# Performance work log

Hardware: AMD Instinct MI355X
Metric: run time of the kernel (lower is better)

The kernel has to match this reference:

```python
import jax, jax.numpy as jnp
import numpy as np

B, N, D, E = 64, 512, 256, 524288
VOCAB, NTYPES = 50000, 8
NUM_NODES = B * N


def setup_inputs() -> dict:
    key = jax.random.key(0)
    ks = jax.random.split(key, 20)
    p = lambda k, shape: jax.random.normal(k, shape, jnp.float32) * 0.05
    return {
        'x_tokens': jax.random.randint(ks[0], (NUM_NODES,), 0, VOCAB),
        'word_type': jax.random.randint(ks[1], (NUM_NODES,), 0, NTYPES),
        'edge_index': jax.random.randint(ks[2], (2, E), 0, NUM_NODES),
        'edge_attr': jax.random.uniform(ks[3], (E,), jnp.float32),
        'mask_pad': jnp.ones((B, N, 1), jnp.float32),
        'mask_score': jnp.zeros((B, N), jnp.float32),
        'emb_table': p(ks[4], (VOCAB, D)),
        'wt_table': p(ks[5], (NTYPES, D)),
        'W_w': p(ks[6], (D, D)), 'b_w': jnp.zeros((D,), jnp.float32),
        'W_g1': p(ks[7], (D, D)), 'b_g1': jnp.zeros((D,), jnp.float32),
        'W_g2': p(ks[8], (D, D)), 'b_g2': jnp.zeros((D,), jnp.float32),
        'W_p1': p(ks[9], (D, D)), 'b_p1': jnp.zeros((D,), jnp.float32),
        'W_p2': p(ks[10], (D, 1)),
        'Wih_x': p(ks[11], (4 * D, D)), 'Whh_x': p(ks[12], (4 * D, D)),
        'bih_x': jnp.zeros((4 * D,), jnp.float32), 'bhh_x': jnp.zeros((4 * D,), jnp.float32),
        'Wih_g': p(ks[13], (4 * D, D)), 'Whh_g': p(ks[14], (4 * D, D)),
        'bih_g': jnp.zeros((4 * D,), jnp.float32), 'bhh_g': jnp.zeros((4 * D,), jnp.float32),
    }


def _lstm_cell(x, h, c, Wih, Whh, bih, bhh):
    g = x @ Wih.T + h @ Whh.T + (bih + bhh)
    i, f, gg, o = jnp.split(g, 4, axis=-1)  # torch gate order: i, f, g, o
    c = jax.nn.sigmoid(f) * c + jax.nn.sigmoid(i) * jnp.tanh(gg)
    h = jax.nn.sigmoid(o) * jnp.tanh(c)
    return h, c


def _lstm_last(x0, x1, Wih, Whh, bih, bhh):
    # batch_first LSTM over seq-len-2 input; return last hidden output
    z = jnp.zeros_like(x0)
    h, c = _lstm_cell(x0, z, z, Wih, Whh, bih, bhh)
    h, _ = _lstm_cell(x1, h, c, Wih, Whh, bih, bhh)
    return h


def _gcn(x, src, dst, ew, W, b):
    # PyG GCNConv with edge_weight: add self-loops (w=1), symmetric norm
    deg = jax.ops.segment_sum(ew, dst, NUM_NODES) + 1.0
    dinv = jax.lax.rsqrt(deg)
    norm = dinv[src] * ew * dinv[dst]  # [E]
    xw = x @ W                         # [NUM_NODES, D]
    out = jax.ops.segment_sum(norm[:, None] * xw[src], dst, NUM_NODES)
    out = out + (dinv * dinv)[:, None] * xw  # self-loop contribution
    return out + b


def _pool(x2d, W_p1, b_p1, W_p2, mask_score):
    x3 = x2d.reshape(B, N, D)
    h = jnp.tanh(x3 @ W_p1 + b_p1)
    score = (h @ W_p2)[..., 0] + mask_score  # [B, N]
    alpha = jax.nn.softmax(score, axis=-1)
    return jnp.sum(alpha[..., None] * x3, axis=1)  # [B, D]


def reference(x_tokens, word_type, edge_index, edge_attr, mask_pad, mask_score,
              emb_table, wt_table, W_w, b_w, W_g1, b_g1, W_g2, b_g2,
              W_p1, b_p1, W_p2, Wih_x, Whh_x, bih_x, bhh_x,
              Wih_g, Whh_g, bih_g, bhh_g):
    src, dst = edge_index[0], edge_index[1]
    x = emb_table[x_tokens] + wt_table[word_type]  # use_wordtype == True
    x = x @ W_w + b_w
    x1_mid = _gcn(x, src, dst, edge_attr, W_g1, b_g1)
    x1 = _lstm_last(x, x1_mid, Wih_x, Whh_x, bih_x, bhh_x)
    g1 = _pool(x1, W_p1, b_p1, W_p2, mask_score)
    x2_mid = _gcn(x1, src, dst, edge_attr, W_g2, b_g2)
    x2 = _lstm_last(x1, x2_mid, Wih_x, Whh_x, bih_x, bhh_x)
    g2 = _pool(x2, W_p1, b_p1, W_p2, mask_score)
    graph_out = _lstm_last(g1, g2, Wih_g, Whh_g, bih_g, bhh_g)  # [B, D]
    x_out = jnp.tanh(x2).reshape(B, N, D) * mask_pad
    return x_out, graph_out
```

## Files before the change

### kernel.cpp

```cpp
#include <hip/hip_runtime.h>
#include <hip/hip_bf16.h>
#include <math.h>

#define NODES 32768
#define DD 256
#define NE 524288
#define BATCH 64
#define SEQ 512

typedef __attribute__((ext_vector_type(8))) short short8v;
typedef __attribute__((ext_vector_type(4))) float f32x4;
typedef unsigned short u16;

__device__ __forceinline__ float sigf(float x) { return 1.0f / (1.0f + expf(-x)); }
__device__ __forceinline__ float bfu(u16 u) {
    unsigned int x = ((unsigned int)u) << 16;
    float f;
    __builtin_memcpy(&f, &x, 4);
    return f;
}
__device__ __forceinline__ u16 f2b(float f) {
    __hip_bfloat16 h = __float2bfloat16(f);
    u16 u;
    __builtin_memcpy(&u, &h, 2);
    return u;
}
__device__ __forceinline__ void split_store(float v, u16* __restrict__ hi, u16* __restrict__ lo, int idx) {
    u16 h = f2b(v);
    hi[idx] = h;
    lo[idx] = f2b(v - bfu(h));
}

__global__ __launch_bounds__(256) void wsplitT(const float* __restrict__ W,
                                               u16* __restrict__ h, u16* __restrict__ l) {
    int n = blockIdx.x, k = threadIdx.x;
    split_store(W[k * 256 + n], h, l, n * 256 + k);
}
__global__ __launch_bounds__(256) void wsplit(const float* __restrict__ W,
                                              u16* __restrict__ h, u16* __restrict__ l) {
    int i = blockIdx.x * 256 + threadIdx.x;
    split_store(W[i], h, l, i);
}

__global__ __launch_bounds__(256) void embed_split(const int* __restrict__ tok,
                                                   const int* __restrict__ wty,
                                                   const float* __restrict__ emb,
                                                   const float* __restrict__ wt,
                                                   u16* __restrict__ xh, u16* __restrict__ xl) {
    int i = blockIdx.x, d = threadIdx.x;
    float v = emb[tok[i] * DD + d] + wt[wty[i] * DD + d];
    split_store(v, xh, xl, i * DD + d);
}

template <bool TANH>
__global__ __launch_bounds__(256) void mfma_gemm(const u16* __restrict__ Ah, const u16* __restrict__ Al,
                                                 const u16* __restrict__ Bh, const u16* __restrict__ Bl,
                                                 const float* __restrict__ bias,
                                                 u16* __restrict__ Chi, u16* __restrict__ Clo) {
    const int l = threadIdx.x & 63, w = threadIdx.x >> 6;
    const int m0 = blockIdx.x * 64, n0 = w * 64;
    const int lr = l & 15, lk = (l >> 4) * 8;
    f32x4 acc[4][4];
#pragma unroll
    for (int mi = 0; mi < 4; ++mi)
#pragma unroll
        for (int ni = 0; ni < 4; ++ni) acc[mi][ni] = (f32x4){0.f, 0.f, 0.f, 0.f};

    const u16* APtr[3] = {Ah, Ah, Al};
    const u16* BPtr[3] = {Bh, Bl, Bh};
    for (int term = 0; term < 3; ++term) {
        const u16* A = APtr[term];
        const u16* B = BPtr[term];
#pragma unroll
        for (int kb = 0; kb < 8; ++kb) {
            int ka = kb * 32 + lk;
            short8v a[4], b[4];
#pragma unroll
            for (int mi = 0; mi < 4; ++mi)
                a[mi] = *(const short8v*)&A[(m0 + mi * 16 + lr) * 256 + ka];
#pragma unroll
            for (int ni = 0; ni < 4; ++ni)
                b[ni] = *(const short8v*)&B[(n0 + ni * 16 + lr) * 256 + ka];
#pragma unroll
            for (int mi = 0; mi < 4; ++mi)
#pragma unroll
                for (int ni = 0; ni < 4; ++ni)
                    acc[mi][ni] = __builtin_amdgcn_mfma_f32_16x16x32_bf16(a[mi], b[ni], acc[mi][ni], 0, 0, 0);
        }
    }
#pragma unroll
    for (int mi = 0; mi < 4; ++mi)
#pragma unroll
        for (int ni = 0; ni < 4; ++ni) {
            int col = n0 + ni * 16 + lr;
            float bs = bias[col];
#pragma unroll
            for (int r = 0; r < 4; ++r) {
                int row = m0 + mi * 16 + (l >> 4) * 4 + r;
                float v = acc[mi][ni][r] + bs;
                if (TANH) v = tanhf(v);
                split_store(v, Chi, Clo, row * 256 + col);
            }
        }
}

template <bool FIRST>
__global__ __launch_bounds__(256) void mfma_lstm(const u16* __restrict__ Xh, const u16* __restrict__ Xl,
                                                 const u16* __restrict__ Hh, const u16* __restrict__ Hl,
                                                 const u16* __restrict__ Wih_h, const u16* __restrict__ Wih_l,
                                                 const u16* __restrict__ Whh_h, const u16* __restrict__ Whh_l,
                                                 const float* __restrict__ bih, const float* __restrict__ bhh,
                                                 const float* __restrict__ c_in, float* __restrict__ c_out,
                                                 u16* __restrict__ Ohi, u16* __restrict__ Olo) {
    __shared__ float lds[4][64][65];
    const int l = threadIdx.x & 63, g = threadIdx.x >> 6;
    const int m0 = blockIdx.x * 64, d0 = blockIdx.y * 64;
    const int lr = l & 15, lk = (l >> 4) * 8;
    f32x4 acc[4][4];
#pragma unroll
    for (int mi = 0; mi < 4; ++mi)
#pragma unroll
        for (int ni = 0; ni < 4; ++ni) acc[mi][ni] = (f32x4){0.f, 0.f, 0.f, 0.f};

    const int npass = FIRST ? 1 : 2;
    for (int pass = 0; pass < npass; ++pass) {
        const u16* Ih = pass ? Hh : Xh;
        const u16* Il = pass ? Hl : Xl;
        const u16* Wh = pass ? Whh_h : Wih_h;
        const u16* Wl = pass ? Whh_l : Wih_l;
        const u16* APtr[3] = {Ih, Ih, Il};
        const u16* BPtr[3] = {Wh, Wl, Wh};
        for (int term = 0; term < 3; ++term) {
            const u16* A = APtr[term];
            const u16* B = BPtr[term];
#pragma unroll
            for (int kb = 0; kb < 8; ++kb) {
                int ka = kb * 32 + lk;
                short8v a[4], b[4];
#pragma unroll
                for (int mi = 0; mi < 4; ++mi)
                    a[mi] = *(const short8v*)&A[(m0 + mi * 16 + lr) * 256 + ka];
#pragma unroll
                for (int ni = 0; ni < 4; ++ni)
                    b[ni] = *(const short8v*)&B[(g * 256 + d0 + ni * 16 + lr) * 256 + ka];
#pragma unroll
                for (int mi = 0; mi < 4; ++mi)
#pragma unroll
                    for (int ni = 0; ni < 4; ++ni)
                        acc[mi][ni] = __builtin_amdgcn_mfma_f32_16x16x32_bf16(a[mi], b[ni], acc[mi][ni], 0, 0, 0);
            }
        }
    }
#pragma unroll
    for (int mi = 0; mi < 4; ++mi)
#pragma unroll
        for (int ni = 0; ni < 4; ++ni)
#pragma unroll
            for (int r = 0; r < 4; ++r)
                lds[g][mi * 16 + (l >> 4) * 4 + r][ni * 16 + lr] = acc[mi][ni][r];
    __syncthreads();
#pragma unroll 4
    for (int rep = 0; rep < 16; ++rep) {
        int idx = rep * 256 + threadIdx.x;
        int ml = idx >> 6, dl = idx & 63;
        int row = m0 + ml, d = d0 + dl;
        float gi = lds[0][ml][dl] + bih[d] + bhh[d];
        float gf = lds[1][ml][dl] + bih[256 + d] + bhh[256 + d];
        float gg = lds[2][ml][dl] + bih[512 + d] + bhh[512 + d];
        float go = lds[3][ml][dl] + bih[768 + d] + bhh[768 + d];
        float cprev = FIRST ? 0.0f : c_in[row * 256 + d];
        float cv = sigf(gf) * cprev + sigf(gi) * tanhf(gg);
        float hv = sigf(go) * tanhf(cv);
        c_out[row * 256 + d] = cv;
        split_store(hv, Ohi, Olo, row * 256 + d);
    }
}

template <bool FIRST>
__global__ __launch_bounds__(256) void lstm_gemm(const float* __restrict__ X,
                                                 const float* __restrict__ H,
                                                 const float* __restrict__ Wih,
                                                 const float* __restrict__ Whh,
                                                 const float* __restrict__ bih,
                                                 const float* __restrict__ bhh,
                                                 const float* __restrict__ c_in,
                                                 float* __restrict__ c_out,
                                                 float* __restrict__ h_out, int M) {
    __shared__ float As[16][68];
    __shared__ float Bs[4][16][68];
    const int m0 = blockIdx.x * 64;
    const int n0 = blockIdx.y * 64;
    const int t = threadIdx.x;
    const int ty = t >> 4, tx = t & 15;
    const int lm = t >> 2;
    const int lk4 = (t & 3) * 4;
    float acc[4][4][4] = {};
    const int npass = FIRST ? 1 : 2;
    for (int pass = 0; pass < npass; ++pass) {
        const float* Ain = pass ? H : X;
        const float* W = pass ? Whh : Wih;
        for (int k0 = 0; k0 < 256; k0 += 16) {
            float4 av = *(const float4*)&Ain[(m0 + lm) * 256 + k0 + lk4];
            float4 w0 = *(const float4*)&W[(0 * 256 + n0 + lm) * 256 + k0 + lk4];
            float4 w1 = *(const float4*)&W[(1 * 256 + n0 + lm) * 256 + k0 + lk4];
            float4 w2 = *(const float4*)&W[(2 * 256 + n0 + lm) * 256 + k0 + lk4];
            float4 w3 = *(const float4*)&W[(3 * 256 + n0 + lm) * 256 + k0 + lk4];
            __syncthreads();
            As[lk4 + 0][lm] = av.x; As[lk4 + 1][lm] = av.y;
            As[lk4 + 2][lm] = av.z; As[lk4 + 3][lm] = av.w;
            Bs[0][lk4 + 0][lm] = w0.x; Bs[0][lk4 + 1][lm] = w0.y;
            Bs[0][lk4 + 2][lm] = w0.z; Bs[0][lk4 + 3][lm] = w0.w;
            Bs[1][lk4 + 0][lm] = w1.x; Bs[1][lk4 + 1][lm] = w1.y;
            Bs[1][lk4 + 2][lm] = w1.z; Bs[1][lk4 + 3][lm] = w1.w;
            Bs[2][lk4 + 0][lm] = w2.x; Bs[2][lk4 + 1][lm] = w2.y;
            Bs[2][lk4 + 2][lm] = w2.z; Bs[2][lk4 + 3][lm] = w2.w;
            Bs[3][lk4 + 0][lm] = w3.x; Bs[3][lk4 + 1][lm] = w3.y;
            Bs[3][lk4 + 2][lm] = w3.z; Bs[3][lk4 + 3][lm] = w3.w;
            __syncthreads();
#pragma unroll
            for (int kk = 0; kk < 16; ++kk) {
                float4 a = *(const float4*)&As[kk][ty * 4];
                float av4[4] = {a.x, a.y, a.z, a.w};
#pragma unroll
                for (int gg = 0; gg < 4; ++gg) {
                    float4 b = *(const float4*)&Bs[gg][kk][tx * 4];
                    float bv4[4] = {b.x, b.y, b.z, b.w};
#pragma unroll
                    for (int i = 0; i < 4; ++i)
#pragma unroll
                        for (int j = 0; j < 4; ++j)
                            acc[gg][i][j] = fmaf(av4[i], bv4[j], acc[gg][i][j]);
                }
            }
        }
    }
#pragma unroll
    for (int i = 0; i < 4; ++i) {
        int r = m0 + ty * 4 + i;
#pragma unroll
        for (int j = 0; j < 4; ++j) {
            int dcol = n0 + tx * 4 + j;
            float gi = acc[0][i][j] + bih[dcol] + bhh[dcol];
            float gf = acc[1][i][j] + bih[256 + dcol] + bhh[256 + dcol];
            float gg = acc[2][i][j] + bih[512 + dcol] + bhh[512 + dcol];
            float go = acc[3][i][j] + bih[768 + dcol] + bhh[768 + dcol];
            float cprev = FIRST ? 0.0f : c_in[r * 256 + dcol];
            float cv = sigf(gf) * cprev + sigf(gi) * tanhf(gg);
            float hv = sigf(go) * tanhf(cv);
            c_out[r * 256 + dcol] = cv;
            h_out[r * 256 + dcol] = hv;
        }
    }
}

__global__ __launch_bounds__(256) void csr_init(int* __restrict__ counts, float* __restrict__ deg) {
    int i = blockIdx.x * 256 + threadIdx.x;
    counts[i] = 0;
    deg[i] = 1.0f;
}
__global__ __launch_bounds__(256) void csr_hist(const int* __restrict__ dst,
                                                const float* __restrict__ ew,
                                                int* __restrict__ counts,
                                                float* __restrict__ deg) {
    int e = blockIdx.x * 256 + threadIdx.x;
    int d = dst[e];
    atomicAdd(&counts[d], 1);
    atomicAdd(&deg[d], ew[e]);
}
__global__ __launch_bounds__(256) void csr_dinv(float* __restrict__ deg) {
    int i = blockIdx.x * 256 + threadIdx.x;
    deg[i] = 1.0f / sqrtf(deg[i]);
}
__global__ __launch_bounds__(256) void csr_scan(const int* __restrict__ counts,
                                                int* __restrict__ offs,
                                                int* __restrict__ cursor) {
    __shared__ int part[256];
    int t = threadIdx.x;
    int base = t * 128;
    int s = 0;
    for (int k = 0; k < 128; ++k) s += counts[base + k];
    part[t] = s;
    __syncthreads();
    for (int off = 1; off < 256; off <<= 1) {
        int v = part[t];
        int add = (t >= off) ? part[t - off] : 0;
        __syncthreads();
        part[t] = v + add;
        __syncthreads();
    }
    int run = part[t] - s;
    for (int k = 0; k < 128; ++k) {
        int c = counts[base + k];
        offs[base + k] = run;
        cursor[base + k] = run;
        run += c;
    }
    if (t == 255) offs[NODES] = run;
}
__global__ __launch_bounds__(256) void csr_fill(const int* __restrict__ src,
                                                const int* __restrict__ dst,
                                                const float* __restrict__ ew,
                                                const float* __restrict__ dinv,
                                                int* __restrict__ cursor,
                                                int* __restrict__ es,
                                                float* __restrict__ en) {
    int e = blockIdx.x * 256 + threadIdx.x;
    int s = src[e], d = dst[e];
    int pos = atomicAdd(&cursor[d], 1);
    es[pos] = s;
    en[pos] = dinv[s] * ew[e] * dinv[d];
}

__global__ __launch_bounds__(256) void gcn_gather(const u16* __restrict__ xh, const u16* __restrict__ xl,
                                                  const int* __restrict__ offs,
                                                  const int* __restrict__ es,
                                                  const float* __restrict__ en,
                                                  const float* __restrict__ dinv,
                                                  u16* __restrict__ oh, u16* __restrict__ ol) {
    int i = blockIdx.x, d = threadIdx.x;
    float di = dinv[i];
    float acc = di * di * (bfu(xh[i * DD + d]) + bfu(xl[i * DD + d]));
    int a = offs[i], b = offs[i + 1];
    for (int j = a; j < b; ++j) {
        int s = es[j];
        float w = en[j];
        acc += w * (bfu(xh[s * DD + d]) + bfu(xl[s * DD + d]));
    }
    split_store(acc, oh, ol, i * DD + d);
}

__global__ __launch_bounds__(256) void score_kernel(const u16* __restrict__ hh, const u16* __restrict__ hl,
                                                    const float* __restrict__ Wp2,
                                                    const float* __restrict__ mask_score,
                                                    float* __restrict__ score) {
    int m = blockIdx.x * 4 + (threadIdx.x >> 6);
    int l = threadIdx.x & 63;
    ushort4 a = *(const ushort4*)&hh[m * DD + l * 4];
    ushort4 b = *(const ushort4*)&hl[m * DD + l * 4];
    float4 w = *(const float4*)&Wp2[l * 4];
    float d = (bfu(a.x) + bfu(b.x)) * w.x + (bfu(a.y) + bfu(b.y)) * w.y +
              (bfu(a.z) + bfu(b.z)) * w.z + (bfu(a.w) + bfu(b.w)) * w.w;
#pragma unroll
    for (int off = 32; off; off >>= 1) d += __shfl_down(d, off);
    if (l == 0) score[m] = d + mask_score[m];
}

__global__ __launch_bounds__(256) void pool_kernel(const u16* __restrict__ xh, const u16* __restrict__ xl,
                                                   const float* __restrict__ score,
                                                   float* __restrict__ gout) {
    int b = blockIdx.x;
    int t = threadIdx.x;
    __shared__ float sal[512];
    __shared__ float wred[4];
    __shared__ float sbc[2];
    int lane = t & 63, wv = t >> 6;
    float s0 = score[b * SEQ + t];
    float s1 = score[b * SEQ + 256 + t];
    float m = fmaxf(s0, s1);
#pragma unroll
    for (int off = 32; off; off >>= 1) m = fmaxf(m, __shfl_down(m, off));
    if (lane == 0) wred[wv] = m;
    __syncthreads();
    if (t == 0) sbc[0] = fmaxf(fmaxf(wred[0], wred[1]), fmaxf(wred[2], wred[3]));
    __syncthreads();
    float mx = sbc[0];
    float e0 = expf(s0 - mx), e1 = expf(s1 - mx);
    sal[t] = e0;
    sal[t + 256] = e1;
    float sm = e0 + e1;
#pragma unroll
    for (int off = 32; off; off >>= 1) sm += __shfl_down(sm, off);
    __syncthreads();
    if (lane == 0) wred[wv] = sm;
    __syncthreads();
    if (t == 0) sbc[1] = wred[0] + wred[1] + wred[2] + wred[3];
    __syncthreads();
    float inv = 1.0f / sbc[1];
    float accv = 0.0f;
    size_t base = (size_t)b * SEQ * DD + t;
    for (int n = 0; n < SEQ; ++n)
        accv += sal[n] * (bfu(xh[base + (size_t)n * DD]) + bfu(xl[base + (size_t)n * DD]));
    gout[b * DD + t] = accv * inv;
}

__global__ __launch_bounds__(256) void final_kernel(const u16* __restrict__ xh, const u16* __restrict__ xl,
                                                    const float* __restrict__ mask_pad,
                                                    float* __restrict__ out) {
    int i = blockIdx.x, d = threadIdx.x;
    float v = bfu(xh[i * DD + d]) + bfu(xl[i * DD + d]);
    out[i * DD + d] = tanhf(v) * mask_pad[i];
}

extern "C" void kernel_launch(void* const* d_in, const int* in_sizes, int n_in,
                              void* d_out, int out_size, void* d_ws, size_t ws_size,
                              hipStream_t stream) {
    const int* x_tokens = (const int*)d_in[0];
    const int* word_type = (const int*)d_in[1];
    const int* edge_src = (const int*)d_in[2];
    const int* edge_dst = edge_src + NE;
    const float* edge_attr = (const float*)d_in[3];
    const float* mask_pad = (const float*)d_in[4];
    const float* mask_score = (const float*)d_in[5];
    const float* emb = (const float*)d_in[6];
    const float* wt = (const float*)d_in[7];
    const float* W_w = (const float*)d_in[8];
    const float* b_w = (const float*)d_in[9];
    const float* W_g1 = (const float*)d_in[10];
    const float* b_g1 = (const float*)d_in[11];
    const float* W_g2 = (const float*)d_in[12];
    const float* b_g2 = (const float*)d_in[13];
    const float* W_p1 = (const float*)d_in[14];
    const float* b_p1 = (const float*)d_in[15];
    const float* W_p2 = (const float*)d_in[16];
    const float* Wih_x = (const float*)d_in[17];
    const float* Whh_x = (const float*)d_in[18];
    const float* bih_x = (const float*)d_in[19];
    const float* bhh_x = (const float*)d_in[20];
    const float* Wih_g = (const float*)d_in[21];
    const float* Whh_g = (const float*)d_in[22];
    const float* bih_g = (const float*)d_in[23];
    const float* bhh_g = (const float*)d_in[24];

    float* out = (float*)d_out;
    char* ws = (char*)d_ws;

    int* counts = (int*)ws;
    int* cursor = counts + NODES;
    int* offs = cursor + NODES;
    float* dinv = (float*)(offs + NODES + 64);
    float* score = dinv + NODES;
    float* g1 = score + NODES;
    float* g2 = g1 + BATCH * DD;
    float* hg = g2 + BATCH * DD;
    float* cg = hg + BATCH * DD;
    int* es = (int*)(cg + BATCH * DD);
    float* en = (float*)(es + NE);
    u16* wsm = (u16*)(en + NE);
    u16* wwTh = wsm;               u16* wwTl = wwTh + 65536;
    u16* wg1h = wwTl + 65536;      u16* wg1l = wg1h + 65536;
    u16* wg2h = wg1l + 65536;      u16* wg2l = wg2h + 65536;
    u16* wp1h = wg2l + 65536;      u16* wp1l = wp1h + 65536;
    u16* wihh = wp1l + 65536;      u16* wihl = wihh + 262144;
    u16* whhh = wihl + 262144;     u16* whhl = whhh + 262144;

    const size_t NDf = (size_t)NODES * DD;
    u16* base = (u16*)(ws + (8u << 20));
    u16* S1h = base;               u16* S1l = S1h + NDf;
    u16* S2h = S1l + NDf;          u16* S2l = S2h + NDf;
    u16* S3h = S2l + NDf;          u16* S3l = S3h + NDf;
    float* OUTB = out;

    dim3 blk(256);
    dim3 gemmGrid(NODES / 64);
    dim3 lstmGrid(NODES / 64, 4);

    csr_init<<<NODES / 256, blk, 0, stream>>>(counts, dinv);
    csr_hist<<<NE / 256, blk, 0, stream>>>(edge_dst, edge_attr, counts, dinv);
    csr_dinv<<<NODES / 256, blk, 0, stream>>>(dinv);
    csr_scan<<<1, blk, 0, stream>>>(counts, offs, cursor);
    csr_fill<<<NE / 256, blk, 0, stream>>>(edge_src, edge_dst, edge_attr, dinv, cursor, es, en);

    wsplitT<<<256, blk, 0, stream>>>(W_w, wwTh, wwTl);
    wsplitT<<<256, blk, 0, stream>>>(W_g1, wg1h, wg1l);
    wsplitT<<<256, blk, 0, stream>>>(W_g2, wg2h, wg2l);
    wsplitT<<<256, blk, 0, stream>>>(W_p1, wp1h, wp1l);
    wsplit<<<1024, blk, 0, stream>>>(Wih_x, wihh, wihl);
    wsplit<<<1024, blk, 0, stream>>>(Whh_x, whhh, whhl);

    embed_split<<<NODES, blk, 0, stream>>>(x_tokens, word_type, emb, wt, S1h, S1l);
    mfma_gemm<false><<<gemmGrid, blk, 0, stream>>>(S1h, S1l, wwTh, wwTl, b_w, S2h, S2l);
    gcn_gather<<<NODES, blk, 0, stream>>>(S2h, S2l, offs, es, en, dinv, S1h, S1l);
    mfma_gemm<false><<<gemmGrid, blk, 0, stream>>>(S1h, S1l, wg1h, wg1l, b_g1, S3h, S3l);
    mfma_lstm<true><<<lstmGrid, blk, 0, stream>>>(S2h, S2l, nullptr, nullptr, wihh, wihl, whhh, whhl,
                                                  bih_x, bhh_x, nullptr, OUTB, S1h, S1l);
    mfma_lstm<false><<<lstmGrid, blk, 0, stream>>>(S3h, S3l, S1h, S1l, wihh, wihl, whhh, whhl,
                                                   bih_x, bhh_x, OUTB, OUTB, S2h, S2l);
    mfma_gemm<true><<<gemmGrid, blk, 0, stream>>>(S2h, S2l, wp1h, wp1l, b_p1, S3h, S3l);
    score_kernel<<<NODES / 4, blk, 0, stream>>>(S3h, S3l, W_p2, mask_score, score);
    pool_kernel<<<BATCH, blk, 0, stream>>>(S2h, S2l, score, g1);
    gcn_gather<<<NODES, blk, 0, stream>>>(S2h, S2l, offs, es, en, dinv, S1h, S1l);
    mfma_gemm<false><<<gemmGrid, blk, 0, stream>>>(S1h, S1l, wg2h, wg2l, b_g2, S3h, S3l);
    mfma_lstm<true><<<lstmGrid, blk, 0, stream>>>(S2h, S2l, nullptr, nullptr, wihh, wihl, whhh, whhl,
                                                  bih_x, bhh_x, nullptr, OUTB, S1h, S1l);
    mfma_lstm<false><<<lstmGrid, blk, 0, stream>>>(S3h, S3l, S1h, S1l, wihh, wihl, whhh, whhl,
                                                   bih_x, bhh_x, OUTB, OUTB, S2h, S2l);
    mfma_gemm<true><<<gemmGrid, blk, 0, stream>>>(S2h, S2l, wp1h, wp1l, b_p1, S3h, S3l);
    score_kernel<<<NODES / 4, blk, 0, stream>>>(S3h, S3l, W_p2, mask_score, score);
    pool_kernel<<<BATCH, blk, 0, stream>>>(S2h, S2l, score, g2);
    lstm_gemm<true><<<dim3(1, 4), blk, 0, stream>>>(g1, nullptr, Wih_g, Whh_g, bih_g, bhh_g,
                                                    nullptr, cg, hg, BATCH);
    lstm_gemm<false><<<dim3(1, 4), blk, 0, stream>>>(g2, hg, Wih_g, Whh_g, bih_g, bhh_g,
                                                     cg, cg, out + NODES * DD, BATCH);
    final_kernel<<<NODES, blk, 0, stream>>>(S2h, S2l, mask_pad, out);
}
```

Baseline: 2.118 ms.

## Give each wave all four LSTM gates for its columns, dropping the LDS epilogue

The MFMA LSTM kernel now assigns each wave a 16-column slice across all four gates instead of one gate per wave. The gate nonlinearities can then be applied directly from registers, with no LDS staging and no __syncthreads. The three split-bf16 terms are also merged into one k-loop, so hi and lo tiles are loaded once per k-step rather than through three separate passes. The trade-off is that weight tiles are read per wave for 16 columns, and more vector registers are live at once.

```diff
diff --git a/kernel.cpp b/kernel.cpp
--- a/kernel.cpp
+++ b/kernel.cpp
@@ -112,15 +112,15 @@
                                                  const float* __restrict__ bih, const float* __restrict__ bhh,
                                                  const float* __restrict__ c_in, float* __restrict__ c_out,
                                                  u16* __restrict__ Ohi, u16* __restrict__ Olo) {
-    __shared__ float lds[4][64][65];
-    const int l = threadIdx.x & 63, g = threadIdx.x >> 6;
-    const int m0 = blockIdx.x * 64, d0 = blockIdx.y * 64;
+    const int l = threadIdx.x & 63, w = threadIdx.x >> 6;
+    const int m0 = blockIdx.x * 64;
+    const int dw = blockIdx.y * 64 + w * 16;
     const int lr = l & 15, lk = (l >> 4) * 8;
     f32x4 acc[4][4];
 #pragma unroll
-    for (int mi = 0; mi < 4; ++mi)
-#pragma unroll
-        for (int ni = 0; ni < 4; ++ni) acc[mi][ni] = (f32x4){0.f, 0.f, 0.f, 0.f};
+    for (int g = 0; g < 4; ++g)
+#pragma unroll
+        for (int mi = 0; mi < 4; ++mi) acc[g][mi] = (f32x4){0.f, 0.f, 0.f, 0.f};
 
     const int npass = FIRST ? 1 : 2;
     for (int pass = 0; pass < npass; ++pass) {
@@ -128,52 +128,50 @@
         const u16* Il = pass ? Hl : Xl;
         const u16* Wh = pass ? Whh_h : Wih_h;
         const u16* Wl = pass ? Whh_l : Wih_l;
-        const u16* APtr[3] = {Ih, Ih, Il};
-        const u16* BPtr[3] = {Wh, Wl, Wh};
-        for (int term = 0; term < 3; ++term) {
-            const u16* A = APtr[term];
-            const u16* B = BPtr[term];
-#pragma unroll
-            for (int kb = 0; kb < 8; ++kb) {
-                int ka = kb * 32 + lk;
-                short8v a[4], b[4];
-#pragma unroll
-                for (int mi = 0; mi < 4; ++mi)
-                    a[mi] = *(const short8v*)&A[(m0 + mi * 16 + lr) * 256 + ka];
-#pragma unroll
-                for (int ni = 0; ni < 4; ++ni)
-                    b[ni] = *(const short8v*)&B[(g * 256 + d0 + ni * 16 + lr) * 256 + ka];
-#pragma unroll
-                for (int mi = 0; mi < 4; ++mi)
-#pragma unroll
-                    for (int ni = 0; ni < 4; ++ni)
-                        acc[mi][ni] = __builtin_amdgcn_mfma_f32_16x16x32_bf16(a[mi], b[ni], acc[mi][ni], 0, 0, 0);
+#pragma unroll
+        for (int kb = 0; kb < 8; ++kb) {
+            int ka = kb * 32 + lk;
+            short8v ah[4], al[4], bh[4], bl[4];
+#pragma unroll
+            for (int mi = 0; mi < 4; ++mi) {
+                ah[mi] = *(const short8v*)&Ih[(m0 + mi * 16 + lr) * 256 + ka];
+                al[mi] = *(const short8v*)&Il[(m0 + mi * 16 + lr) * 256 + ka];
             }
-        }
-    }
+#pragma unroll
+            for (int g = 0; g < 4; ++g) {
+                bh[g] = *(const short8v*)&Wh[(g * 256 + dw + lr) * 256 + ka];
+                bl[g] = *(const short8v*)&Wl[(g * 256 + dw + lr) * 256 + ka];
+            }
+#pragma unroll
+            for (int g = 0; g < 4; ++g)
+#pragma unroll
+                for (int mi = 0; mi < 4; ++mi) {
+                    acc[g][mi] = __builtin_amdgcn_mfma_f32_16x16x32_bf16(al[mi], bh[g], acc[g][mi], 0, 0, 0);
+                    acc[g][mi] = __builtin_amdgcn_mfma_f32_16x16x32_bf16(ah[mi], bl[g], acc[g][mi], 0, 0, 0);
+                    acc[g][mi] = __builtin_amdgcn_mfma_f32_16x16x32_bf16(ah[mi], bh[g], acc[g][mi], 0, 0, 0);
+                }
+        }
+    }
+    const int d = dw + lr;
+    const float bi0 = bih[d] + bhh[d];
+    const float bi1 = bih[256 + d] + bhh[256 + d];
+    const float bi2 = bih[512 + d] + bhh[512 + d];
+    const float bi3 = bih[768 + d] + bhh[768 + d];
 #pragma unroll
     for (int mi = 0; mi < 4; ++mi)
 #pragma unroll
-        for (int ni = 0; ni < 4; ++ni)
-#pragma unroll
-            for (int r = 0; r < 4; ++r)
-                lds[g][mi * 16 + (l >> 4) * 4 + r][ni * 16 + lr] = acc[mi][ni][r];
-    __syncthreads();
-#pragma unroll 4
-    for (int rep = 0; rep < 16; ++rep) {
-        int idx = rep * 256 + threadIdx.x;
-        int ml = idx >> 6, dl = idx & 63;
-        int row = m0 + ml, d = d0 + dl;
-        float gi = lds[0][ml][dl] + bih[d] + bhh[d];
-        float gf = lds[1][ml][dl] + bih[256 + d] + bhh[256 + d];
-        float gg = lds[2][ml][dl] + bih[512 + d] + bhh[512 + d];
-        float go = lds[3][ml][dl] + bih[768 + d] + bhh[768 + d];
-        float cprev = FIRST ? 0.0f : c_in[row * 256 + d];
-        float cv = sigf(gf) * cprev + sigf(gi) * tanhf(gg);
-        float hv = sigf(go) * tanhf(cv);
-        c_out[row * 256 + d] = cv;
-        split_store(hv, Ohi, Olo, row * 256 + d);
-    }
+        for (int r = 0; r < 4; ++r) {
+            int row = m0 + mi * 16 + (l >> 4) * 4 + r;
+            float gi = acc[0][mi][r] + bi0;
+            float gf = acc[1][mi][r] + bi1;
+            float gg = acc[2][mi][r] + bi2;
+            float go = acc[3][mi][r] + bi3;
+            float cprev = FIRST ? 0.0f : c_in[row * 256 + d];
+            float cv = sigf(gf) * cprev + sigf(gi) * tanhf(gg);
+            float hv = sigf(go) * tanhf(cv);
+            c_out[row * 256 + d] = cv;
+            split_store(hv, Ohi, Olo, row * 256 + d);
+        }
 }
 
 template <bool FIRST>
```

Result: faster. 1.852 ms (-12.5%).
